# Kernel tuning notes

Measured on AMD Instinct MI355X. Metric: run time of the kernel, lower is better.

Reference implementation:

```python
import jax, jax.numpy as jnp
import numpy as np

MAX_K_QK = 64
MAX_K_V = 64
MAX_K_KNOW = 128


def threshold_gate(scores, tau, max_k):
    # scores: [B,S,N], tau: [B,S,1]
    raw = scores - tau
    gate = jnp.where(raw > 0, raw, 1e-08 * jnp.exp(raw))
    exp_gate = jnp.exp(gate) - 1.0
    k = min(max_k, scores.shape[-1])
    topk_vals, _ = jax.lax.top_k(exp_gate, k)
    threshold = topk_vals[:, :, -1:]
    exp_gate = jnp.where(exp_gate >= threshold, exp_gate, 0.0)
    gate_sum = exp_gate.sum(axis=-1, keepdims=True) + 1e-08
    gate_strength = jnp.tanh(exp_gate.max(axis=-1, keepdims=True))
    return exp_gate / gate_sum * gate_strength


def setup_inputs() -> dict:
    key = jax.random.key(0)
    ks = jax.random.split(key, 8)
    B, S, D = 2, 2048, 1024
    N_QK, N_V, N_KNOW = 4096, 4096, 8192
    scale = 0.02  # keep scores in a sane range for exp()
    return {
        "x": jax.random.normal(ks[0], (B, S, D), jnp.float32),
        "qk_emb": jax.random.normal(ks[1], (N_QK, D), jnp.float32) * scale,
        "v_emb": jax.random.normal(ks[2], (N_V, D), jnp.float32) * scale,
        "know_emb": jax.random.normal(ks[3], (N_KNOW, D), jnp.float32) * scale,
        "w_attn": jax.random.normal(ks[4], (D, 3), jnp.float32) * scale,
        "b_attn": jnp.zeros((3,), jnp.float32),
        "w_know": jax.random.normal(ks[5], (D, 1), jnp.float32) * scale,
        "b_know": jnp.zeros((1,), jnp.float32),
    }


def reference(x, qk_emb, v_emb, know_emb, w_attn, b_attn, w_know, b_know):
    # deterministic=True -> router dropout is identity
    # attention gates
    scores_qk = jnp.einsum("bsd,nd->bsn", x, qk_emb)
    scores_v = jnp.einsum("bsd,nd->bsn", x, v_emb)
    tau_all = x @ w_attn + b_attn  # [B,S,3]
    g_Q = threshold_gate(scores_qk, tau_all[:, :, 0:1], MAX_K_QK)
    g_K = threshold_gate(scores_qk, tau_all[:, :, 1:2], MAX_K_QK)
    g_V = threshold_gate(scores_v, tau_all[:, :, 2:3], MAX_K_V)
    t_qk = 1.0 / qk_emb.shape[0]
    t_v = 1.0 / v_emb.shape[0]
    aux_attn = (
        ((g_Q.mean(axis=(0, 1)) - t_qk) ** 2).sum() * g_Q.shape[-1]
        + ((g_K.mean(axis=(0, 1)) - t_qk) ** 2).sum() * g_K.shape[-1]
        + ((g_V.mean(axis=(0, 1)) - t_v) ** 2).sum() * g_V.shape[-1]
    )
    # knowledge gates
    scores_know = jnp.einsum("bsd,nd->bsn", x, know_emb)
    tau_know = x @ w_know + b_know  # [B,S,1]
    g_know = threshold_gate(scores_know, tau_know, MAX_K_KNOW)
    t_know = 1.0 / know_emb.shape[0]
    aux_know = ((g_know.mean(axis=(0, 1)) - t_know) ** 2).sum() * g_know.shape[-1]
    return (g_Q, g_K, g_V, aux_attn, g_know, aux_know)
```

## Files before the change

### kernel.cpp

```cpp
#include <hip/hip_runtime.h>
#include <hip/hip_bf16.h>


#define M_ROWS 4096
#define DIM    1024
#define N_QK   4096
#define N_KNOW 8192

typedef unsigned short ushortT;
typedef __attribute__((ext_vector_type(8)))  short short8;
typedef __attribute__((ext_vector_type(16))) float f32x16;

__global__ __launch_bounds__(256) void tau_kernel(
    const float* __restrict__ x, const float* __restrict__ w_attn,
    const float* __restrict__ b_attn, const float* __restrict__ w_know,
    const float* __restrict__ b_know, float* __restrict__ tau4, int D)
{
    __shared__ float s_f[4][4];
    const int row = blockIdx.x;
    const int tid = threadIdx.x;
    const float* xr = x + (size_t)row * D;
    float p0 = 0.f, p1 = 0.f, p2 = 0.f, p3 = 0.f;
    for (int d = tid; d < D; d += 256) {
        float xv = xr[d];
        p0 += xv * w_attn[d * 3 + 0];
        p1 += xv * w_attn[d * 3 + 1];
        p2 += xv * w_attn[d * 3 + 2];
        p3 += xv * w_know[d];
    }
#pragma unroll
    for (int o = 32; o > 0; o >>= 1) {
        p0 += __shfl_down(p0, o, 64);
        p1 += __shfl_down(p1, o, 64);
        p2 += __shfl_down(p2, o, 64);
        p3 += __shfl_down(p3, o, 64);
    }
    const int lane = tid & 63, wv = tid >> 6;
    if (lane == 0) { s_f[wv][0] = p0; s_f[wv][1] = p1; s_f[wv][2] = p2; s_f[wv][3] = p3; }
    __syncthreads();
    if (tid < 4) {
        float v = s_f[0][tid] + s_f[1][tid] + s_f[2][tid] + s_f[3][tid];
        v += (tid < 3) ? b_attn[tid] : b_know[0];
        tau4[(size_t)row * 4 + tid] = v;
    }
}

__device__ __forceinline__ void split4(const float4 v, uint2& H, uint2& L) {
    float vv[4] = {v.x, v.y, v.z, v.w};
    unsigned h[4], l[4];
#pragma unroll
    for (int i = 0; i < 4; i++) {
        __hip_bfloat16 hb = __float2bfloat16(vv[i]);
        float r = vv[i] - __bfloat162float(hb);
        __hip_bfloat16 lb = __float2bfloat16(r);
        h[i] = *(ushortT*)&hb;
        l[i] = *(ushortT*)&lb;
    }
    H.x = h[0] | (h[1] << 16); H.y = h[2] | (h[3] << 16);
    L.x = l[0] | (l[1] << 16); L.y = l[2] | (l[3] << 16);
}

__global__ __launch_bounds__(256) void convertA(
    const float* __restrict__ src, ushortT* __restrict__ dst, int nElem4)
{
    int g = blockIdx.x * 256 + threadIdx.x;
    if (g >= nElem4) return;
    int row = g >> 8;
    int c4  = g & 255;
    int chunk = c4 >> 3, pos = c4 & 7;
    const float4 v = *(const float4*)(src + (size_t)row * DIM + c4 * 4);
    uint2 H, L;
    split4(v, H, L);
    ushortT* base = dst + (size_t)row * 2048 + chunk * 64;
    *(uint2*)(base + pos * 4)      = H;
    *(uint2*)(base + 32 + pos * 4) = L;
}

__global__ __launch_bounds__(512, 2) void gemm_fused4(
    const ushortT* __restrict__ Aext, const ushortT* __restrict__ Bext,
    float* __restrict__ gQ, float* __restrict__ gV, float* __restrict__ gKn,
    int nb0)
{
    extern __shared__ ushortT lds[];
#define ABUF(b) (lds + (b) * 32768)
#define BBUF(b) (lds + (b) * 32768 + 16384)
    const int tid = threadIdx.x;
    const int wave = tid >> 6, lane = tid & 63;
    const int l32 = lane & 31, h = lane >> 5;
    const int rx7 = l32 & 7;
    const int wm = (wave >> 2) * 128;
    const int wn = (wave & 3) * 64;
    const long long m0 = (long long)blockIdx.y * 256;
    const int nblk = nb0 + blockIdx.x;

    float* C; long long ldc; long long n0;
    if (nblk < 16)      { C = gQ;  ldc = N_QK;   n0 = (long long)nblk * 256; }
    else if (nblk < 32) { C = gV;  ldc = N_QK;   n0 = (long long)(nblk - 16) * 256; }
    else                { C = gKn; ldc = N_KNOW; n0 = (long long)(nblk - 32) * 256; }

    const ushortT* gAp[4]; const ushortT* gBp[4]; int lOff[4];
#pragma unroll
    for (int it = 0; it < 4; ++it) {
        int f = it * 512 + tid;
        int r = f >> 3, sp = f & 7;
        int sg = sp ^ (r & 7);
        gAp[it] = Aext + (m0 + r) * 2048 + sg * 8;
        gBp[it] = Bext + ((long long)blockIdx.x * 256 + r) * 2048 + sg * 8;
        lOff[it] = f * 8;
    }

    f32x16 acc[4][2] = {};

#define STAGE(buf, c) do {                                                         \
    _Pragma("unroll")                                                              \
    for (int it = 0; it < 4; ++it) {                                               \
        __builtin_amdgcn_global_load_lds(                                          \
            (const __attribute__((address_space(1))) unsigned*)(const void*)(gAp[it] + (c) * 64), \
            (__attribute__((address_space(3))) unsigned*)(void*)(ABUF(buf) + lOff[it]), 16, 0, 0); \
        __builtin_amdgcn_global_load_lds(                                          \
            (const __attribute__((address_space(1))) unsigned*)(const void*)(gBp[it] + (c) * 64), \
            (__attribute__((address_space(3))) unsigned*)(void*)(BBUF(buf) + lOff[it]), 16, 0, 0); \
    }                                                                              \
} while (0)

#define COMPUTE(buf) do {                                                          \
    _Pragma("unroll")                                                              \
    for (int kb = 0; kb < 2; ++kb) {                                               \
        const int so = ((kb * 2 + h) ^ rx7) * 16;                                  \
        short8 aH[4], aL[4], bH[2], bL[2];                                         \
        _Pragma("unroll")                                                          \
        for (int t = 0; t < 4; ++t) {                                              \
            const char* pa = (const char*)ABUF(buf) + (wm + t * 32 + l32) * 128;   \
            aH[t] = *(const short8*)(pa + so);                                     \
            aL[t] = *(const short8*)(pa + (so ^ 64));                              \
        }                                                                          \
        _Pragma("unroll")                                                          \
        for (int t = 0; t < 2; ++t) {                                              \
            const char* pb = (const char*)BBUF(buf) + (wn + t * 32 + l32) * 128;   \
            bH[t] = *(const short8*)(pb + so);                                     \
            bL[t] = *(const short8*)(pb + (so ^ 64));                              \
        }                                                                          \
        _Pragma("unroll")                                                          \
        for (int i = 0; i < 4; ++i)                                                \
            _Pragma("unroll")                                                      \
            for (int j = 0; j < 2; ++j) {                                          \
                acc[i][j] = __builtin_amdgcn_mfma_f32_32x32x16_bf16(aH[i], bH[j], acc[i][j], 0, 0, 0); \
                acc[i][j] = __builtin_amdgcn_mfma_f32_32x32x16_bf16(aH[i], bL[j], acc[i][j], 0, 0, 0); \
                acc[i][j] = __builtin_amdgcn_mfma_f32_32x32x16_bf16(aL[i], bH[j], acc[i][j], 0, 0, 0); \
                acc[i][j] = __builtin_amdgcn_mfma_f32_32x32x16_bf16(aL[i], bL[j], acc[i][j], 0, 0, 0); \
            }                                                                      \
    }                                                                              \
} while (0)

    STAGE(0, 0);
    __syncthreads();

    for (int c = 0; c < 32; c += 2) {
        STAGE(1, c + 1);
        COMPUTE(0);
        __syncthreads();
        if (c + 2 < 32) STAGE(0, c + 2);
        COMPUTE(1);
        __syncthreads();
    }
#undef STAGE
#undef COMPUTE
#undef ABUF
#undef BBUF

#pragma unroll
    for (int ti = 0; ti < 4; ++ti)
#pragma unroll
        for (int tj = 0; tj < 2; ++tj) {
            long long col = n0 + wn + tj * 32 + l32;
            long long rb  = m0 + wm + ti * 32 + 4 * h;
#pragma unroll
            for (int reg = 0; reg < 16; ++reg) {
                long long row = rb + (reg & 3) + 8 * (reg >> 2);
                C[row * ldc + col] = acc[ti][tj][reg];
            }
        }
}

__global__ __launch_bounds__(256) void gemm_fused2(
    const ushortT* __restrict__ Aext, const float* __restrict__ qk_emb,
    const float* __restrict__ v_emb, const float* __restrict__ know_emb,
    float* __restrict__ gQ, float* __restrict__ gV, float* __restrict__ gKn,
    long long rowOff)
{
    __shared__ ushortT AHL[128 * 64];
    __shared__ ushortT BHL[128 * 64];
    const int tid = threadIdx.x;
    const int wave = tid >> 6, lane = tid & 63;
    const int l32 = lane & 31, h = lane >> 5;
    const int rx7 = l32 & 7;
    const int wm = (wave >> 1) * 64, wn = (wave & 1) * 64;
    const long long m0 = (long long)blockIdx.y * 128;
    const int nblk = blockIdx.x;

    const float* Bsrc; float* C; long long ldc; long long n0;
    if (nblk < 32)      { Bsrc = qk_emb;   C = gQ;  ldc = N_QK;   n0 = (long long)nblk * 128; }
    else if (nblk < 64) { Bsrc = v_emb;    C = gV;  ldc = N_QK;   n0 = (long long)(nblk - 32) * 128; }
    else                { Bsrc = know_emb; C = gKn; ldc = N_KNOW; n0 = (long long)(nblk - 64) * 128; }

    const ushortT* gAp[4]; ushortT* lAp[4];
    const float*   gBp[4]; int offH[4], offL[4];
#pragma unroll
    for (int it = 0; it < 4; ++it) {
        int f = it * 256 + tid;
        int r = f >> 3, sp = f & 7;
        int sg = sp ^ (r & 7);
        gAp[it] = Aext + (m0 + r) * 2048 + sg * 8;
        lAp[it] = AHL + f * 8;
        int c4 = f & 7;
        int s = c4 >> 1, hf = c4 & 1;
        offH[it] = r * 128 + ((s ^ (r & 7)) * 16) + hf * 8;
        offL[it] = r * 128 + (((4 | s) ^ (r & 7)) * 16) + hf * 8;
        gBp[it] = Bsrc + (n0 + r) * DIM + c4 * 4;
    }
    const char* pA[2]; const char* pB[2];
#pragma unroll
    for (int t = 0; t < 2; ++t) {
        pA[t] = (const char*)AHL + (wm + t * 32 + l32) * 128;
        pB[t] = (const char*)BHL + (wn + t * 32 + l32) * 128;
    }

    f32x16 acc[2][2] = {};
    float4 bufB[4];
#pragma unroll
    for (int it = 0; it < 4; ++it) bufB[it] = *(const float4*)(gBp[it]);

    for (int c = 0; c < 32; ++c) {
#pragma unroll
        for (int it = 0; it < 4; ++it) {
            __builtin_amdgcn_global_load_lds(
                (const __attribute__((address_space(1))) unsigned*)(const void*)(gAp[it] + c * 64),
                (__attribute__((address_space(3))) unsigned*)(void*)lAp[it], 16, 0, 0);
            uint2 H, L;
            split4(bufB[it], H, L);
            *(uint2*)((char*)BHL + offH[it]) = H;
            *(uint2*)((char*)BHL + offL[it]) = L;
        }
        __syncthreads();
        if (c + 1 < 32) {
#pragma unroll
            for (int it = 0; it < 4; ++it)
                bufB[it] = *(const float4*)(gBp[it] + (c + 1) * 32);
        }
#pragma unroll
        for (int kb = 0; kb < 2; ++kb) {
            const int so = ((kb * 2 + h) ^ rx7) * 16;
            short8 aH[2], aL[2], bH[2], bL[2];
#pragma unroll
            for (int t = 0; t < 2; ++t) {
                aH[t] = *(const short8*)(pA[t] + so);
                aL[t] = *(const short8*)(pA[t] + (so ^ 64));
                bH[t] = *(const short8*)(pB[t] + so);
                bL[t] = *(const short8*)(pB[t] + (so ^ 64));
            }
#pragma unroll
            for (int i = 0; i < 2; ++i)
#pragma unroll
                for (int j = 0; j < 2; ++j) {
                    acc[i][j] = __builtin_amdgcn_mfma_f32_32x32x16_bf16(aH[i], bH[j], acc[i][j], 0, 0, 0);
                    acc[i][j] = __builtin_amdgcn_mfma_f32_32x32x16_bf16(aH[i], bL[j], acc[i][j], 0, 0, 0);
                    acc[i][j] = __builtin_amdgcn_mfma_f32_32x32x16_bf16(aL[i], bH[j], acc[i][j], 0, 0, 0);
                    acc[i][j] = __builtin_amdgcn_mfma_f32_32x32x16_bf16(aL[i], bL[j], acc[i][j], 0, 0, 0);
                }
        }
        __syncthreads();
    }
#pragma unroll
    for (int ti = 0; ti < 2; ++ti)
#pragma unroll
        for (int tj = 0; tj < 2; ++tj) {
            long long col = n0 + wn + tj * 32 + l32;
            long long rb  = rowOff + m0 + wm + ti * 32 + 4 * h;
#pragma unroll
            for (int reg = 0; reg < 16; ++reg) {
                long long row = rb + (reg & 3) + 8 * (reg >> 2);
                C[row * ldc + col] = acc[ti][tj][reg];
            }
        }
}

__device__ __forceinline__ unsigned floatToKey(float f) {
    unsigned b = __float_as_uint(f);
    return (b & 0x80000000u) ? ~b : (b | 0x80000000u);
}
__device__ __forceinline__ float keyToFloat(unsigned key) {
    unsigned b = (key & 0x80000000u) ? (key & 0x7FFFFFFFu) : ~key;
    return __uint_as_float(b);
}
__device__ __forceinline__ float egate(float raw) {
    float g = raw > 0.f ? raw : 1e-8f * __expf(raw);
    return expf(g) - 1.f;
}

template <int NV, bool VLOAD, bool VSTORE>
__device__ __forceinline__ void gate_body(
    const float* __restrict__ srow, float tA, float tB, bool hasB, int ksel,
    float* __restrict__ orowA, float* __restrict__ orowB,
    float* __restrict__ colA, float* __restrict__ colB,
    int* s_hist, unsigned* s_u, float* s_f)
{
    const int tid = threadIdx.x, lane = tid & 63, wv = tid >> 6;

    unsigned keys[NV * 4];
    unsigned kmax = 0u;
#pragma unroll
    for (int i = 0; i < NV; i++) {
        float v0, v1, v2, v3;
        if (VLOAD) {
            float4 v = *(const float4*)(srow + (size_t)(i * 256 + tid) * 4);
            v0 = v.x; v1 = v.y; v2 = v.z; v3 = v.w;
        } else {
            v0 = srow[(i * 4 + 0) * 256 + tid];
            v1 = srow[(i * 4 + 1) * 256 + tid];
            v2 = srow[(i * 4 + 2) * 256 + tid];
            v3 = srow[(i * 4 + 3) * 256 + tid];
        }
        unsigned a = floatToKey(v0), b = floatToKey(v1);
        unsigned c = floatToKey(v2), d = floatToKey(v3);
        keys[i * 4 + 0] = a; keys[i * 4 + 1] = b;
        keys[i * 4 + 2] = c; keys[i * 4 + 3] = d;
        unsigned m1 = a > b ? a : b, m2 = c > d ? c : d;
        m1 = m1 > m2 ? m1 : m2;
        kmax = kmax > m1 ? kmax : m1;
    }
#pragma unroll
    for (int o = 32; o > 0; o >>= 1) {
        unsigned x = __shfl_down(kmax, o, 64);
        kmax = kmax > x ? kmax : x;
    }
    if (lane == 0) s_u[wv] = kmax;
    __syncthreads();
    { unsigned a = s_u[0], b = s_u[1], c = s_u[2], d = s_u[3];
      unsigned m1 = a > b ? a : b, m2 = c > d ? c : d; kmax = m1 > m2 ? m1 : m2; }
    __syncthreads();

    unsigned prefix = 0u;
    int kk = ksel;
#pragma unroll
    for (int rnd = 0; rnd < 4; ++rnd) {
        const int sh = 24 - 8 * rnd;
        s_hist[tid] = 0;
        __syncthreads();
#pragma unroll
        for (int i = 0; i < NV * 4; i++) {
            unsigned key = keys[i];
            if ((((key ^ prefix) >> sh) >> 8) == 0u)
                atomicAdd(&s_hist[(key >> sh) & 255u], 1);
        }
        __syncthreads();
        if (tid < 64) {
            const int b3 = 255 - 4 * tid;
            const int h0 = s_hist[b3],     h1 = s_hist[b3 - 1];
            const int h2 = s_hist[b3 - 2], h3 = s_hist[b3 - 3];
            const int gsum = h0 + h1 + h2 + h3;
            int inc = gsum;
#pragma unroll
            for (int o = 1; o < 64; o <<= 1) {
                int v = __shfl_up(inc, o, 64);
                if (tid >= o) inc += v;
            }
            const int above = inc - gsum;
            const int c0 = above + h0, c1 = c0 + h1, c2 = c1 + h2, c3 = c2 + h3;
            if (kk > above && kk <= c3) {
                unsigned byt; int nk;
                if (kk <= c0)      { byt = (unsigned)b3;       nk = kk - above; }
                else if (kk <= c1) { byt = (unsigned)(b3 - 1); nk = kk - c0; }
                else if (kk <= c2) { byt = (unsigned)(b3 - 2); nk = kk - c1; }
                else               { byt = (unsigned)(b3 - 3); nk = kk - c2; }
                s_u[0] = byt; s_u[1] = (unsigned)nk;
            }
        }
        __syncthreads();
        prefix |= s_u[0] << sh;
        kk = (int)s_u[1];
    }
    const unsigned vk = prefix;

    float sA = 0.f, sB = 0.f;
#pragma unroll
    for (int i = 0; i < NV * 4; i++) {
        if (keys[i] >= vk) {
            float s = keyToFloat(keys[i]);
            sA += egate(s - tA);
            if (hasB) sB += egate(s - tB);
        }
    }
#pragma unroll
    for (int o = 32; o > 0; o >>= 1) {
        sA += __shfl_down(sA, o, 64);
        sB += __shfl_down(sB, o, 64);
    }
    if (lane == 0) { s_f[wv] = sA; s_f[4 + wv] = sB; }
    __syncthreads();
    sA = s_f[0] + s_f[1] + s_f[2] + s_f[3];
    sB = s_f[4] + s_f[5] + s_f[6] + s_f[7];

    const float smax = keyToFloat(kmax);
    const float scaleA = tanhf(egate(smax - tA)) / (sA + 1e-8f);
    const float scaleB = hasB ? tanhf(egate(smax - tB)) / (sB + 1e-8f) : 0.f;

#pragma unroll
    for (int i = 0; i < NV; i++) {
        float ga[4], gb[4];
        int eidx[4];
#pragma unroll
        for (int j = 0; j < 4; j++) {
            int ii = i * 4 + j;
            int idx = VLOAD ? (i * 1024 + tid * 4 + j) : (ii * 256 + tid);
            eidx[j] = idx;
            unsigned key = keys[ii];
            float vA = 0.f, vB = 0.f;
            if (key >= vk) {
                float s = keyToFloat(key);
                vA = egate(s - tA) * scaleA;
                atomicAdd(&colA[idx], vA);
                if (hasB) { vB = egate(s - tB) * scaleB; atomicAdd(&colB[idx], vB); }
            }
            ga[j] = vA; gb[j] = vB;
        }
        if (VSTORE) {
            *(float4*)(orowA + (size_t)eidx[0]) = make_float4(ga[0], ga[1], ga[2], ga[3]);
            if (hasB) *(float4*)(orowB + (size_t)eidx[0]) = make_float4(gb[0], gb[1], gb[2], gb[3]);
        } else {
#pragma unroll
            for (int j = 0; j < 4; j++) {
                orowA[eidx[j]] = ga[j];
                if (hasB) orowB[eidx[j]] = gb[j];
            }
        }
    }
}

__global__ __launch_bounds__(256) void gate_all(
    const float* __restrict__ tau4,
    float* __restrict__ gQ, float* __restrict__ gK,
    float* __restrict__ gV, float* __restrict__ gKn,
    float* __restrict__ colsums)
{
    __shared__ int s_hist[256];
    __shared__ unsigned s_u[4];
    __shared__ float s_f[8];
    const int bid = blockIdx.x;
    if (bid < 4096) {
        const int row = bid;
        const float t = tau4[(size_t)row * 4 + 3];
        gate_body<8, false, false>(
            gKn + (size_t)row * N_KNOW, t, 0.f, false, 128,
            gKn + (size_t)row * N_KNOW, nullptr,
            colsums + 3 * N_QK, nullptr, s_hist, s_u, s_f);
    } else if (bid < 8192) {
        const int row = bid - 4096;
        const float tA = tau4[(size_t)row * 4 + 0];
        const float tB = tau4[(size_t)row * 4 + 1];
        gate_body<4, true, true>(
            gQ + (size_t)row * N_QK, tA, tB, true, 64,
            gQ + (size_t)row * N_QK, gK + (size_t)row * N_QK,
            colsums, colsums + N_QK, s_hist, s_u, s_f);
    } else {
        const int row = bid - 8192;
        const float t = tau4[(size_t)row * 4 + 2];
        gate_body<4, true, true>(
            gV + (size_t)row * N_QK, t, 0.f, false, 64,
            gV + (size_t)row * N_QK, nullptr,
            colsums + 2 * N_QK, nullptr, s_hist, s_u, s_f);
    }
}

__global__ __launch_bounds__(256) void aux_kernel(
    const float* __restrict__ colsum,
    float* __restrict__ auxAttn, float* __restrict__ auxKnow)
{
    __shared__ float s_a[4];
    __shared__ float s_b[4];
    const int tid = threadIdx.x;
    const int lane = tid & 63, wv = tid >> 6;
    const float invM = 1.f / 4096.f;

    float sa = 0.f;
    const float tqk = 1.f / 4096.f;
    for (int i = tid; i < 3 * N_QK; i += 256) {
        float m = colsum[i] * invM - tqk;
        sa += m * m;
    }
    float sk = 0.f;
    const float tkn = 1.f / 8192.f;
    for (int i = tid; i < N_KNOW; i += 256) {
        float m = colsum[3 * N_QK + i] * invM - tkn;
        sk += m * m;
    }
#pragma unroll
    for (int o = 32; o > 0; o >>= 1) {
        sa += __shfl_down(sa, o, 64);
        sk += __shfl_down(sk, o, 64);
    }
    if (lane == 0) { s_a[wv] = sa; s_b[wv] = sk; }
    __syncthreads();
    if (tid == 0) {
        auxAttn[0] = (s_a[0] + s_a[1] + s_a[2] + s_a[3]) * 4096.f;
        auxKnow[0] = (s_b[0] + s_b[1] + s_b[2] + s_b[3]) * 8192.f;
    }
}

static void convert_b_range(const float* qk, const float* v, const float* kn,
                            ushortT* Bext, long long rowLo, long long rowHi,
                            hipStream_t stream)
{
    struct Seg { const float* p; long long lo, hi; };
    Seg seg[3] = { {qk, 0, 4096}, {v, 4096, 8192}, {kn, 8192, 16384} };
    for (int i = 0; i < 3; ++i) {
        long long lo = rowLo > seg[i].lo ? rowLo : seg[i].lo;
        long long hi = rowHi < seg[i].hi ? rowHi : seg[i].hi;
        if (lo < hi) {
            int nel4 = (int)((hi - lo) * 256);
            convertA<<<(nel4 + 255) / 256, 256, 0, stream>>>(
                seg[i].p + (size_t)(lo - seg[i].lo) * DIM,
                Bext + (size_t)(lo - rowLo) * 2048, nel4);
        }
    }
}

extern "C" void kernel_launch(void* const* d_in, const int* in_sizes, int n_in,
                              void* d_out, int out_size, void* d_ws, size_t ws_size,
                              hipStream_t stream)
{
    const float* x        = (const float*)d_in[0];
    const float* qk_emb   = (const float*)d_in[1];
    const float* v_emb    = (const float*)d_in[2];
    const float* know_emb = (const float*)d_in[3];
    const float* w_attn   = (const float*)d_in[4];
    const float* b_attn   = (const float*)d_in[5];
    const float* w_know   = (const float*)d_in[6];
    const float* b_know   = (const float*)d_in[7];
    float* out = (float*)d_out;

    const long long M = M_ROWS;

    float* gQ   = out;
    float* gK   = gQ + (size_t)M * N_QK;
    float* gV   = gK + (size_t)M * N_QK;
    float* auxA = gV + (size_t)M * N_QK;
    float* gKn  = auxA + 1;
    float* auxK = gKn + (size_t)M * N_KNOW;

    const long long nColsum = 3 * N_QK + N_KNOW;
    const long long tail_bytes = (M * 4 + nColsum) * 4;
    long long tailStart = ((long long)ws_size - tail_bytes) & ~255LL;
    float* tau4 = (float*)((char*)d_ws + tailStart);
    float* colsums = tau4 + (size_t)M * 4;

    const long long rowB = 4096;
    const long long aBytes = M * rowB;

    hipMemsetAsync(colsums, 0, nColsum * sizeof(float), stream);
    tau_kernel<<<(int)M, 256, 0, stream>>>(x, w_attn, b_attn, w_know, b_know, tau4, DIM);

    long long availB = tailStart - aBytes;
    long long nbc = availB > 0 ? availB / (256 * rowB) : 0;
    if (nbc > 64) nbc = 64;

    if (nbc >= 16) {
        ushortT* A_ext = (ushortT*)d_ws;
        ushortT* B_ext = (ushortT*)((char*)d_ws + aBytes);
        convertA<<<(int)(M * 256 / 256), 256, 0, stream>>>(x, A_ext, (int)(M * 256));
        for (long long nb0 = 0; nb0 < 64; nb0 += nbc) {
            long long nn = (64 - nb0 < nbc) ? (64 - nb0) : nbc;
            convert_b_range(qk_emb, v_emb, know_emb, B_ext,
                            nb0 * 256, (nb0 + nn) * 256, stream);
            gemm_fused4<<<dim3((unsigned)nn, 16), 512, 131072, stream>>>(
                A_ext, B_ext, gQ, gV, gKn, (int)nb0);
        }
    } else {
        long long ra = (tailStart / rowB / 128) * 128;
        if (ra > M) ra = M;
        if (ra < 128) ra = 128;
        ushortT* A_ext = (ushortT*)d_ws;
        for (long long a0 = 0; a0 < M; a0 += ra) {
            long long ac = (M - a0 < ra) ? (M - a0) : ra;
            int nel4 = (int)(ac * 256);
            convertA<<<(nel4 + 255) / 256, 256, 0, stream>>>(x + a0 * DIM, A_ext, nel4);
            gemm_fused2<<<dim3(128, (unsigned)(ac / 128)), 256, 0, stream>>>(
                A_ext, qk_emb, v_emb, know_emb, gQ, gV, gKn, a0);
        }
    }

    gate_all<<<12288, 256, 0, stream>>>(tau4, gQ, gK, gV, gKn, colsums);

    aux_kernel<<<1, 256, 0, stream>>>(colsums, auxA, auxK);
}
```

Measured before the change: 968.4 us.

## Prefilter radix-select histogram with mean+2σ pivot and restructure GEMM barrier pipeline

The GEMM main loop now prefetches two stages ahead. It uses explicit vmcnt waits and raw s_barrier/sched_barrier, replacing the previous __syncthreads ping-pong, so global loads overlap compute with less synchronisation. In the top-k gate, each row computes its mean and standard deviation along with the max and counts keys above mean+2σ. If at least k keys pass, the radix-select histogram rounds skip keys below that pivot, which cuts LDS atomic traffic. This adds an extra reduction and barrier per row. The filter stays exact because it falls back to no filtering when too few keys pass.

```diff
diff --git a/kernel.cpp b/kernel.cpp
--- a/kernel.cpp
+++ b/kernel.cpp
@@ -153,15 +153,17 @@
 } while (0)
 
     STAGE(0, 0);
-    __syncthreads();
-
-    for (int c = 0; c < 32; c += 2) {
-        STAGE(1, c + 1);
-        COMPUTE(0);
-        __syncthreads();
-        if (c + 2 < 32) STAGE(0, c + 2);
-        COMPUTE(1);
-        __syncthreads();
+    STAGE(1, 1);
+
+    for (int c = 0; c < 32; ++c) {
+        if (c < 31) asm volatile("s_waitcnt vmcnt(8)" ::: "memory");
+        else        asm volatile("s_waitcnt vmcnt(0)" ::: "memory");
+        __builtin_amdgcn_s_barrier();
+        __builtin_amdgcn_sched_barrier(0);
+        COMPUTE(c & 1);
+        __builtin_amdgcn_s_barrier();
+        __builtin_amdgcn_sched_barrier(0);
+        if (c + 2 < 32) STAGE(c & 1, c + 2);
     }
 #undef STAGE
 #undef COMPUTE
@@ -308,6 +310,7 @@
 
     unsigned keys[NV * 4];
     unsigned kmax = 0u;
+    float fs = 0.f, fq = 0.f;
 #pragma unroll
     for (int i = 0; i < NV; i++) {
         float v0, v1, v2, v3;
@@ -320,6 +323,8 @@
             v2 = srow[(i * 4 + 2) * 256 + tid];
             v3 = srow[(i * 4 + 3) * 256 + tid];
         }
+        fs += v0 + v1 + v2 + v3;
+        fq += v0 * v0 + v1 * v1 + v2 * v2 + v3 * v3;
         unsigned a = floatToKey(v0), b = floatToKey(v1);
         unsigned c = floatToKey(v2), d = floatToKey(v3);
         keys[i * 4 + 0] = a; keys[i * 4 + 1] = b;
@@ -332,12 +337,31 @@
     for (int o = 32; o > 0; o >>= 1) {
         unsigned x = __shfl_down(kmax, o, 64);
         kmax = kmax > x ? kmax : x;
-    }
-    if (lane == 0) s_u[wv] = kmax;
+        fs += __shfl_down(fs, o, 64);
+        fq += __shfl_down(fq, o, 64);
+    }
+    if (lane == 0) { s_u[wv] = kmax; s_f[wv] = fs; s_f[4 + wv] = fq; }
     __syncthreads();
     { unsigned a = s_u[0], b = s_u[1], c = s_u[2], d = s_u[3];
       unsigned m1 = a > b ? a : b, m2 = c > d ? c : d; kmax = m1 > m2 ? m1 : m2; }
+    fs = s_f[0] + s_f[1] + s_f[2] + s_f[3];
+    fq = s_f[4] + s_f[5] + s_f[6] + s_f[7];
+
+    const float NT = (float)(NV * 4 * 256);
+    const float mu = fs / NT;
+    const float sd = sqrtf(fmaxf(fq / NT - mu * mu, 0.f));
+    const unsigned pk = floatToKey(mu + 2.0f * sd);
     __syncthreads();
+
+    int pc = 0;
+#pragma unroll
+    for (int i = 0; i < NV * 4; i++) pc += (keys[i] >= pk) ? 1 : 0;
+#pragma unroll
+    for (int o = 32; o > 0; o >>= 1) pc += __shfl_down(pc, o, 64);
+    if (lane == 0) s_u[wv] = (unsigned)pc;
+    __syncthreads();
+    const int ptot = (int)(s_u[0] + s_u[1] + s_u[2] + s_u[3]);
+    const unsigned filt = (ptot >= ksel) ? pk : 0u;
 
     unsigned prefix = 0u;
     int kk = ksel;
@@ -349,7 +373,7 @@
 #pragma unroll
         for (int i = 0; i < NV * 4; i++) {
             unsigned key = keys[i];
-            if ((((key ^ prefix) >> sh) >> 8) == 0u)
+            if (key >= filt && (((key ^ prefix) >> sh) >> 8) == 0u)
                 atomicAdd(&s_hist[(key >> sh) & 255u], 1);
         }
         __syncthreads();
```

After: 959.1 us, median of 2. About the same (-1.0%).
